# Kernel tuning notes

Measured on AMD Instinct MI355X. Metric: run time of the kernel, lower is better.

## Reference

```python
import jax, jax.numpy as jnp
import numpy as np

B, H, W, C = 2, 256, 256, 96
NH, WS, SS = 3, 8, 4
HD = C // NH
N = WS * WS              # tokens per window
NWIMG = (H // WS) * (W // WS)  # windows per image
MLP = 4 * C
EPS = 1e-5

def _np_attn_mask():
    img = np.zeros((H, W))
    sl = (slice(0, -WS), slice(-WS, -SS), slice(-SS, None))
    cnt = 0
    for a in sl:
        for b in sl:
            img[a, b] = cnt
            cnt += 1
    m = img.reshape(H // WS, WS, W // WS, WS).transpose(0, 2, 1, 3).reshape(-1, N)
    am = m[:, None, :] - m[:, :, None]
    return np.where(am != 0, -100.0, 0.0).astype(np.float32)

def _np_rel_index():
    coords = np.stack(np.meshgrid(np.arange(WS), np.arange(WS), indexing='ij'))
    cf = coords.reshape(2, -1)
    rel = (cf[:, :, None] - cf[:, None, :]).transpose(1, 2, 0).copy()
    rel[..., 0] += WS - 1
    rel[..., 1] += WS - 1
    rel[..., 0] *= 2 * WS - 1
    return rel.sum(-1)

def _np_coords_table():
    r = np.arange(-(WS - 1), WS, dtype=np.float32)
    t = np.stack(np.meshgrid(r, r, indexing='ij'), axis=-1) / (WS - 1) * 8.0
    t = np.sign(t) * np.log2(np.abs(t) + 1.0) / np.log2(8.0)
    return t.reshape(-1, 2)

ATTN_MASK = jnp.asarray(_np_attn_mask())          # [NWIMG, N, N]
REL_INDEX = jnp.asarray(_np_rel_index().reshape(-1))
COORDS_TABLE = jnp.asarray(_np_coords_table())    # [(2WS-1)^2, 2]

def setup_inputs():
    key = jax.random.key(0)
    ks = jax.random.split(key, 16)
    s = 0.02
    return {
        'hidden_states': jax.random.normal(ks[0], (B, H * W, C), jnp.float32),
        'time': jax.random.uniform(ks[1], (B,), jnp.float32),
        'q_w': jax.random.normal(ks[2], (C, C), jnp.float32) * s,
        'q_b': jnp.zeros((C,), jnp.float32),
        'k_w': jax.random.normal(ks[3], (C, C), jnp.float32) * s,
        'v_w': jax.random.normal(ks[4], (C, C), jnp.float32) * s,
        'v_b': jnp.zeros((C,), jnp.float32),
        'proj_w': jax.random.normal(ks[5], (C, C), jnp.float32) * s,
        'proj_b': jnp.zeros((C,), jnp.float32),
        'logit_scale': jnp.full((NH, 1, 1), jnp.log(10.0), jnp.float32),
        'cpb_w1': jax.random.normal(ks[6], (2, 512), jnp.float32) * s,
        'cpb_b1': jnp.zeros((512,), jnp.float32),
        'cpb_w2': jax.random.normal(ks[7], (512, NH), jnp.float32) * s,
        'lnb_ww': jax.random.normal(ks[8], (1, C), jnp.float32) * s,
        'lnb_wb': jnp.ones((C,), jnp.float32),
        'lnb_bw': jax.random.normal(ks[9], (1, C), jnp.float32) * s,
        'lnb_bb': jnp.zeros((C,), jnp.float32),
        'lna_ww': jax.random.normal(ks[10], (1, C), jnp.float32) * s,
        'lna_wb': jnp.ones((C,), jnp.float32),
        'lna_bw': jax.random.normal(ks[11], (1, C), jnp.float32) * s,
        'lna_bb': jnp.zeros((C,), jnp.float32),
        'fc1_w': jax.random.normal(ks[12], (C, MLP), jnp.float32) * s,
        'fc1_b': jnp.zeros((MLP,), jnp.float32),
        'fc2_w': jax.random.normal(ks[13], (MLP, C), jnp.float32) * s,
        'fc2_b': jnp.zeros((C,), jnp.float32),
    }

def _cln(x, time, ww, wb, bw, bb):
    # ConditionalLayerNorm: stats over channels, affine params from time via Linear(1, C)
    mean = x.mean(-1, keepdims=True)
    var = (x * x).mean(-1, keepdims=True) - mean * mean
    xn = (x - mean) / jnp.sqrt(var + EPS)
    t = time.reshape(-1, 1)
    w = (t @ ww + wb)[:, None, :]
    b = (t @ bw + bb)[:, None, :]
    return w * xn + b

def reference(hidden_states, time, q_w, q_b, k_w, v_w, v_b, proj_w, proj_b, logit_scale, cpb_w1, cpb_b1, cpb_w2, lnb_ww, lnb_wb, lnb_bw, lnb_bb, lna_ww, lna_wb, lna_bw, lna_bb, fc1_w, fc1_b, fc2_w, fc2_b):
    shortcut = hidden_states
    x = hidden_states.reshape(B, H, W, C)
    x = jnp.roll(x, (-SS, -SS), axis=(1, 2))  # cyclic shift
    # window partition -> [nW, N, C]
    xw = x.reshape(B, H // WS, WS, W // WS, WS, C).transpose(0, 1, 3, 2, 4, 5).reshape(-1, N, C)
    nW = B * NWIMG
    q = (xw @ q_w + q_b).reshape(nW, N, NH, HD).transpose(0, 2, 1, 3)
    k = (xw @ k_w).reshape(nW, N, NH, HD).transpose(0, 2, 1, 3)  # key has no bias in Swinv2
    v = (xw @ v_w + v_b).reshape(nW, N, NH, HD).transpose(0, 2, 1, 3)
    # cosine attention with clamped learnable log temperature
    qn = q / jnp.maximum(jnp.linalg.norm(q, axis=-1, keepdims=True), 1e-12)
    kn = k / jnp.maximum(jnp.linalg.norm(k, axis=-1, keepdims=True), 1e-12)
    scale = jnp.exp(jnp.minimum(logit_scale, jnp.log(100.0)))  # [NH,1,1]
    attn = jnp.einsum('whnd,whmd->whnm', qn, kn) * scale[None]
    # continuous relative position bias: MLP(2->512->NH) over log-spaced coords
    bias_table = jax.nn.relu(COORDS_TABLE @ cpb_w1 + cpb_b1) @ cpb_w2
    bias = bias_table[REL_INDEX].reshape(N, N, NH).transpose(2, 0, 1)
    attn = attn + 16.0 * jax.nn.sigmoid(bias)[None]
    # shifted-window mask
    attn = attn.reshape(B, NWIMG, NH, N, N) + ATTN_MASK[None, :, None]
    attn = jax.nn.softmax(attn.reshape(nW, NH, N, N), axis=-1)
    ctx = jnp.einsum('whnm,whmd->whnd', attn, v).transpose(0, 2, 1, 3).reshape(nW, N, C)
    ctx = ctx @ proj_w + proj_b
    # window reverse + un-shift
    xr = ctx.reshape(B, H // WS, W // WS, WS, WS, C).transpose(0, 1, 3, 2, 4, 5).reshape(B, H, W, C)
    xr = jnp.roll(xr, (SS, SS), axis=(1, 2))
    attn_out = xr.reshape(B, H * W, C)
    # post-norm residual (Swin v2 style) with conditional LN
    hs = shortcut + _cln(attn_out, time, lnb_ww, lnb_wb, lnb_bw, lnb_bb)
    inter = jax.nn.gelu(hs @ fc1_w + fc1_b, approximate=False)
    mlp_out = inter @ fc2_w + fc2_b
    return hs + _cln(mlp_out, time, lna_ww, lna_wb, lna_bw, lna_bb)
```

## Files before the change

kernel.cpp:

```cpp
#include <hip/hip_runtime.h>
#include <hip/hip_bf16.h>

typedef __bf16 bf16_t;
typedef bf16_t bf16x8 __attribute__((ext_vector_type(8)));
typedef bf16_t bf16x4 __attribute__((ext_vector_type(4)));
typedef float  f32x4  __attribute__((ext_vector_type(4)));

#define LDC 104
#define LDT 72

#define WS_WQ    0
#define WS_WK    19968
#define WS_WV    39936
#define WS_WP    59904
#define WS_FC1   79872
#define WS_FC2   159744
#define WS_BIAS  239616

__device__ __forceinline__ f32x4 mfma16(bf16x8 a, bf16x8 b, f32x4 c) {
    return __builtin_amdgcn_mfma_f32_16x16x32_bf16(a, b, c, 0, 0, 0);
}

__device__ __forceinline__ float cpbf(int v) {
    float x = (float)v * (8.0f / 7.0f);
    float l = log2f(fabsf(x) + 1.0f) * (1.0f / 3.0f);
    return x < 0.f ? -l : l;
}

__device__ __forceinline__ int regcnt(int t, int hw, int ww) {
    int r = t >> 3, c = t & 7;
    int rr = (hw == 31) ? (r < 4 ? 1 : 2) : 0;
    int cc = (ww == 31) ? (c < 4 ? 1 : 2) : 0;
    return rr * 3 + cc;
}

__global__ __launch_bounds__(256) void k0_prep(
    const float* __restrict__ qw, const float* __restrict__ kw,
    const float* __restrict__ vw, const float* __restrict__ pw,
    const float* __restrict__ fc1w, const float* __restrict__ fc2w,
    const float* __restrict__ cw1, const float* __restrict__ cb1,
    const float* __restrict__ cw2, char* __restrict__ ws)
{
    int tid = threadIdx.x;
    if (blockIdx.x == 0) {
        __shared__ float table[225 * 3];
        if (tid < 225) {
            int ia = tid / 15, ib = tid % 15;
            float c0 = cpbf(ia - 7), c1 = cpbf(ib - 7);
            float a0 = 0.f, a1 = 0.f, a2 = 0.f;
            for (int j = 0; j < 512; ++j) {
                float h = fmaf(c0, cw1[j], fmaf(c1, cw1[512 + j], cb1[j]));
                h = fmaxf(h, 0.f);
                a0 = fmaf(h, cw2[j * 3 + 0], a0);
                a1 = fmaf(h, cw2[j * 3 + 1], a1);
                a2 = fmaf(h, cw2[j * 3 + 2], a2);
            }
            table[tid * 3 + 0] = a0; table[tid * 3 + 1] = a1; table[tid * 3 + 2] = a2;
        }
        __syncthreads();
        float* bias = (float*)(ws + WS_BIAS);
        for (int e = tid; e < 3 * 64 * 64; e += 256) {
            int h = e >> 12, nm = e & 4095, n = nm >> 6, m = nm & 63;
            int dr = (n >> 3) - (m >> 3) + 7, dc = (n & 7) - (m & 7) + 7;
            float t = table[(dr * 15 + dc) * 3 + h];
            bias[e] = 16.f / (1.f + __expf(-t));
        }
    } else {
        int idx = (blockIdx.x - 1) * 256 + tid;
        if (idx < 36864) {
            int which = idx / 9216, r = idx % 9216;
            int o = r / 96, i = r % 96;
            const float* src = which == 0 ? qw : which == 1 ? kw : which == 2 ? vw : pw;
            ((bf16_t*)(ws + WS_WQ + which * 19968))[o * LDC + i] = (bf16_t)src[i * 96 + o];
        } else if (idx < 73728) {
            int r = idx - 36864;
            int o = r / 96, i = r % 96;
            ((bf16_t*)(ws + WS_FC1))[o * LDC + i] = (bf16_t)fc1w[i * 384 + o];
        } else if (idx < 110592) {
            int r = idx - 73728;
            int ks = r / 9216, rr = r % 9216, o = rr / 96, j = rr % 96;
            ((bf16_t*)(ws + WS_FC2))[(ks * 96 + o) * LDC + j] = (bf16_t)fc2w[(ks * 96 + j) * 96 + o];
        }
    }
}

__global__ __launch_bounds__(256) void kA_attn(
    const float* __restrict__ hidden, const float* __restrict__ tv,
    const float* __restrict__ qb, const float* __restrict__ vb,
    const float* __restrict__ pb, const float* __restrict__ lsc,
    const float* __restrict__ lnww, const float* __restrict__ lnwb,
    const float* __restrict__ lnbw, const float* __restrict__ lnbb,
    const char* __restrict__ ws, float* __restrict__ hs)
{
    __shared__ __align__(16) char sm[73728];
    bf16_t* xwb   = (bf16_t*)(sm + 0);
    bf16_t* wbuf  = (bf16_t*)(sm + 13312);
    bf16_t* qn    = (bf16_t*)(sm + 33280);
    bf16_t* kn    = (bf16_t*)(sm + 46592);
    bf16_t* vT    = (bf16_t*)(sm + 59904);
    bf16_t* P     = (bf16_t*)(sm + 0);
    bf16_t* ctxb  = (bf16_t*)(sm + 33280);
    bf16_t* wbuf2 = (bf16_t*)(sm + 46592);

    const int tid = threadIdx.x;
    const int wv = tid >> 6, lane = tid & 63, lg = lane >> 4, lr = lane & 15;
    const int wid = blockIdx.x;
    const int bat = wid >> 10, wim = wid & 1023, hw = wim >> 5, wwi = wim & 31;

    #pragma unroll
    for (int i = 0; i < 6; ++i) {
        int idx = tid + 256 * i;
        int t = idx / 24, grp = idx % 24;
        int gr = ((hw << 3) + (t >> 3) + 4) & 255;
        int gc = ((wwi << 3) + (t & 7) + 4) & 255;
        const float4 v = *(const float4*)(hidden + (((size_t)bat << 16) + (gr << 8) + gc) * 96 + grp * 4);
        bf16x4 p; p[0] = (bf16_t)v.x; p[1] = (bf16_t)v.y; p[2] = (bf16_t)v.z; p[3] = (bf16_t)v.w;
        *(bf16x4*)(xwb + t * LDC + grp * 4) = p;
    }
    {
        const float4* s4 = (const float4*)(ws + WS_WQ);
        float4* d4 = (float4*)wbuf;
        for (int i = tid; i < 1248; i += 256) d4[i] = s4[i];
    }
    __syncthreads();

    {
        bf16x8 af[3];
        #pragma unroll
        for (int ks = 0; ks < 3; ++ks) af[ks] = *(const bf16x8*)(xwb + (16 * wv + lr) * LDC + 32 * ks + 8 * lg);
        f32x4 acc[6];
        #pragma unroll
        for (int nt = 0; nt < 6; ++nt) {
            f32x4 a = {0.f, 0.f, 0.f, 0.f};
            #pragma unroll
            for (int ks = 0; ks < 3; ++ks)
                a = mfma16(af[ks], *(const bf16x8*)(wbuf + (16 * nt + lr) * LDC + 32 * ks + 8 * lg), a);
            float bq = qb[16 * nt + lr];
            #pragma unroll
            for (int j = 0; j < 4; ++j) a[j] += bq;
            acc[nt] = a;
        }
        #pragma unroll
        for (int h = 0; h < 3; ++h) {
            #pragma unroll
            for (int j = 0; j < 4; ++j) {
                float s = acc[2 * h][j] * acc[2 * h][j] + acc[2 * h + 1][j] * acc[2 * h + 1][j];
                s += __shfl_xor(s, 1); s += __shfl_xor(s, 2); s += __shfl_xor(s, 4); s += __shfl_xor(s, 8);
                float inv = 1.f / fmaxf(sqrtf(s), 1e-12f);
                int row = 16 * wv + 4 * lg + j;
                qn[row * LDC + 32 * h + lr]      = (bf16_t)(acc[2 * h][j] * inv);
                qn[row * LDC + 32 * h + 16 + lr] = (bf16_t)(acc[2 * h + 1][j] * inv);
            }
        }
    }
    __syncthreads();
    { const float4* s4 = (const float4*)(ws + WS_WK); float4* d4 = (float4*)wbuf;
      for (int i = tid; i < 1248; i += 256) d4[i] = s4[i]; }
    __syncthreads();

    {
        bf16x8 af[3];
        #pragma unroll
        for (int ks = 0; ks < 3; ++ks) af[ks] = *(const bf16x8*)(xwb + (16 * wv + lr) * LDC + 32 * ks + 8 * lg);
        f32x4 acc[6];
        #pragma unroll
        for (int nt = 0; nt < 6; ++nt) {
            f32x4 a = {0.f, 0.f, 0.f, 0.f};
            #pragma unroll
            for (int ks = 0; ks < 3; ++ks)
                a = mfma16(af[ks], *(const bf16x8*)(wbuf + (16 * nt + lr) * LDC + 32 * ks + 8 * lg), a);
            acc[nt] = a;
        }
        #pragma unroll
        for (int h = 0; h < 3; ++h) {
            #pragma unroll
            for (int j = 0; j < 4; ++j) {
                float s = acc[2 * h][j] * acc[2 * h][j] + acc[2 * h + 1][j] * acc[2 * h + 1][j];
                s += __shfl_xor(s, 1); s += __shfl_xor(s, 2); s += __shfl_xor(s, 4); s += __shfl_xor(s, 8);
                float inv = 1.f / fmaxf(sqrtf(s), 1e-12f);
                int row = 16 * wv + 4 * lg + j;
                kn[row * LDC + 32 * h + lr]      = (bf16_t)(acc[2 * h][j] * inv);
                kn[row * LDC + 32 * h + 16 + lr] = (bf16_t)(acc[2 * h + 1][j] * inv);
            }
        }
    }
    __syncthreads();
    { const float4* s4 = (const float4*)(ws + WS_WV); float4* d4 = (float4*)wbuf;
      for (int i = tid; i < 1248; i += 256) d4[i] = s4[i]; }
    __syncthreads();

    {
        bf16x8 af[3];
        #pragma unroll
        for (int ks = 0; ks < 3; ++ks) af[ks] = *(const bf16x8*)(xwb + (16 * wv + lr) * LDC + 32 * ks + 8 * lg);
        #pragma unroll
        for (int nt = 0; nt < 6; ++nt) {
            f32x4 a = {0.f, 0.f, 0.f, 0.f};
            #pragma unroll
            for (int ks = 0; ks < 3; ++ks)
                a = mfma16(af[ks], *(const bf16x8*)(wbuf + (16 * nt + lr) * LDC + 32 * ks + 8 * lg), a);
            int col = 16 * nt + lr;
            float bv = vb[col];
            bf16x4 pk;
            #pragma unroll
            for (int j = 0; j < 4; ++j) pk[j] = (bf16_t)(a[j] + bv);
            *(bf16x4*)(vT + col * LDT + 16 * wv + 4 * lg) = pk;
        }
    }
    __syncthreads();

    {
        float ls[3];
        #pragma unroll
        for (int h = 0; h < 3; ++h) ls[h] = __expf(fminf(lsc[h], 4.6051702f));
        f32x4 s[3][4];
        #pragma unroll
        for (int h = 0; h < 3; ++h) {
            bf16x8 aq = *(const bf16x8*)(qn + (16 * wv + lr) * LDC + 32 * h + 8 * lg);
            #pragma unroll
            for (int f = 0; f < 4; ++f) {
                f32x4 z = {0.f, 0.f, 0.f, 0.f};
                s[h][f] = mfma16(aq, *(const bf16x8*)(kn + (16 * f + lr) * LDC + 32 * h + 8 * lg), z);
            }
        }
        const float* biasT = (const float*)(ws + WS_BIAS);
        int cntm[4], cnti[4];
        #pragma unroll
        for (int f = 0; f < 4; ++f) cntm[f] = regcnt(16 * f + lr, hw, wwi);
        #pragma unroll
        for (int j = 0; j < 4; ++j) cnti[j] = regcnt(16 * wv + 4 * lg + j, hw, wwi);
        #pragma unroll
        for (int h = 0; h < 3; ++h) {
            #pragma unroll
            for (int f = 0; f < 4; ++f) {
                #pragma unroll
                for (int j = 0; j < 4; ++j) {
                    float b = biasT[(h << 12) + (16 * wv + 4 * lg + j) * 64 + 16 * f + lr];
                    float mk = (cnti[j] != cntm[f]) ? -100.f : 0.f;
                    s[h][f][j] = fmaf(s[h][f][j], ls[h], b + mk);
                }
            }
            #pragma unroll
            for (int j = 0; j < 4; ++j) {
                float mx = fmaxf(fmaxf(s[h][0][j], s[h][1][j]), fmaxf(s[h][2][j], s[h][3][j]));
                mx = fmaxf(mx, __shfl_xor(mx, 1)); mx = fmaxf(mx, __shfl_xor(mx, 2));
                mx = fmaxf(mx, __shfl_xor(mx, 4)); mx = fmaxf(mx, __shfl_xor(mx, 8));
                float sum = 0.f;
                #pragma unroll
                for (int f = 0; f < 4; ++f) { float e = __expf(s[h][f][j] - mx); s[h][f][j] = e; sum += e; }
                sum += __shfl_xor(sum, 1); sum += __shfl_xor(sum, 2); sum += __shfl_xor(sum, 4); sum += __shfl_xor(sum, 8);
                float inv = 1.f / sum;
                int row = 16 * wv + 4 * lg + j;
                #pragma unroll
                for (int f = 0; f < 4; ++f)
                    P[h * 64 * LDT + row * LDT + 16 * f + lr] = (bf16_t)(s[h][f][j] * inv);
            }
        }
    }
    __syncthreads();

    {
        f32x4 ctx[6]; f32x4 zz = {0.f, 0.f, 0.f, 0.f};
        #pragma unroll
        for (int t = 0; t < 6; ++t) ctx[t] = zz;
        #pragma unroll
        for (int h = 0; h < 3; ++h) {
            #pragma unroll
            for (int ks = 0; ks < 2; ++ks) {
                bf16x8 ap = *(const bf16x8*)(P + h * 64 * LDT + (16 * wv + lr) * LDT + 32 * ks + 8 * lg);
                #pragma unroll
                for (int dt = 0; dt < 2; ++dt)
                    ctx[2 * h + dt] = mfma16(ap, *(const bf16x8*)(vT + (32 * h + 16 * dt + lr) * LDT + 32 * ks + 8 * lg), ctx[2 * h + dt]);
            }
        }
        #pragma unroll
        for (int t = 0; t < 6; ++t) {
            #pragma unroll
            for (int j = 0; j < 4; ++j)
                ctxb[(16 * wv + 4 * lg + j) * LDC + 16 * t + lr] = (bf16_t)ctx[t][j];
        }
    }
    __syncthreads();
    { const float4* s4 = (const float4*)(ws + WS_WP); float4* d4 = (float4*)wbuf2;
      for (int i = tid; i < 1248; i += 256) d4[i] = s4[i]; }
    __syncthreads();

    {
        bf16x8 af[3];
        #pragma unroll
        for (int ks = 0; ks < 3; ++ks) af[ks] = *(const bf16x8*)(ctxb + (16 * wv + lr) * LDC + 32 * ks + 8 * lg);
        f32x4 acc[6];
        #pragma unroll
        for (int nt = 0; nt < 6; ++nt) {
            f32x4 a = {0.f, 0.f, 0.f, 0.f};
            #pragma unroll
            for (int ks = 0; ks < 3; ++ks)
                a = mfma16(af[ks], *(const bf16x8*)(wbuf2 + (16 * nt + lr) * LDC + 32 * ks + 8 * lg), a);
            float bp = pb[16 * nt + lr];
            #pragma unroll
            for (int j = 0; j < 4; ++j) a[j] += bp;
            acc[nt] = a;
        }
        float tb = tv[bat];
        #pragma unroll
        for (int j = 0; j < 4; ++j) {
            float smn = 0.f, sq = 0.f;
            #pragma unroll
            for (int t = 0; t < 6; ++t) { float v = acc[t][j]; smn += v; sq = fmaf(v, v, sq); }
            smn += __shfl_xor(smn, 1); smn += __shfl_xor(smn, 2); smn += __shfl_xor(smn, 4); smn += __shfl_xor(smn, 8);
            sq  += __shfl_xor(sq, 1);  sq  += __shfl_xor(sq, 2);  sq  += __shfl_xor(sq, 4);  sq  += __shfl_xor(sq, 8);
            float mean = smn * (1.f / 96.f);
            float var  = sq * (1.f / 96.f) - mean * mean;
            float rstd = rsqrtf(var + 1e-5f);
            int trow = 16 * wv + 4 * lg + j;
            int gr = ((hw << 3) + (trow >> 3) + 4) & 255;
            int gc = ((wwi << 3) + (trow & 7) + 4) & 255;
            size_t gbase = (((size_t)bat << 16) + (gr << 8) + gc) * 96;
            #pragma unroll
            for (int t = 0; t < 6; ++t) {
                int col = 16 * t + lr;
                float w = fmaf(tb, lnww[col], lnwb[col]);
                float b = fmaf(tb, lnbw[col], lnbb[col]);
                float xn = (acc[t][j] - mean) * rstd;
                hs[gbase + col] = hidden[gbase + col] + fmaf(w, xn, b);
            }
        }
    }
}

__global__ __launch_bounds__(256) void kB_mlp(
    const float* __restrict__ tv, const float* __restrict__ fc1b,
    const float* __restrict__ fc2b,
    const float* __restrict__ lnww, const float* __restrict__ lnwb,
    const float* __restrict__ lnbw, const float* __restrict__ lnbb,
    const char* __restrict__ ws, float* __restrict__ io)
{
    __shared__ __align__(16) char sm[66560];
    bf16_t* hsb  = (bf16_t*)(sm + 0);
    bf16_t* w1c  = (bf16_t*)(sm + 13312);
    bf16_t* gbuf = (bf16_t*)(sm + 33280);
    bf16_t* w2c  = (bf16_t*)(sm + 46592);

    const int tid = threadIdx.x;
    const int wv = tid >> 6, lane = tid & 63, lg = lane >> 4, lr = lane & 15;
    const size_t t0 = (size_t)blockIdx.x * 64;

    #pragma unroll
    for (int i = 0; i < 6; ++i) {
        int idx = tid + 256 * i;
        int t = idx / 24, grp = idx % 24;
        const float4 v = *(const float4*)(io + (t0 + t) * 96 + grp * 4);
        bf16x4 p; p[0] = (bf16_t)v.x; p[1] = (bf16_t)v.y; p[2] = (bf16_t)v.z; p[3] = (bf16_t)v.w;
        *(bf16x4*)(hsb + t * LDC + grp * 4) = p;
    }
    __syncthreads();

    f32x4 mlp[6]; f32x4 zz = {0.f, 0.f, 0.f, 0.f};
    #pragma unroll
    for (int t = 0; t < 6; ++t) mlp[t] = zz;
    bf16x8 hf[3];
    #pragma unroll
    for (int ks = 0; ks < 3; ++ks) hf[ks] = *(const bf16x8*)(hsb + (16 * wv + lr) * LDC + 32 * ks + 8 * lg);

    for (int ch = 0; ch < 4; ++ch) {
        { const float4* s1 = (const float4*)(ws + WS_FC1 + ch * 19968);
          const float4* s2 = (const float4*)(ws + WS_FC2 + ch * 19968);
          float4* d1 = (float4*)w1c; float4* d2 = (float4*)w2c;
          for (int i = tid; i < 1248; i += 256) { d1[i] = s1[i]; d2[i] = s2[i]; } }
        __syncthreads();
        #pragma unroll
        for (int nt = 0; nt < 6; ++nt) {
            f32x4 a = {0.f, 0.f, 0.f, 0.f};
            #pragma unroll
            for (int ks = 0; ks < 3; ++ks)
                a = mfma16(hf[ks], *(const bf16x8*)(w1c + (16 * nt + lr) * LDC + 32 * ks + 8 * lg), a);
            float bb = fc1b[ch * 96 + 16 * nt + lr];
            #pragma unroll
            for (int j = 0; j < 4; ++j) {
                float x = a[j] + bb;
                float g = 0.5f * x * (1.f + erff(x * 0.70710678f));
                gbuf[(16 * wv + 4 * lg + j) * LDC + 16 * nt + lr] = (bf16_t)g;
            }
        }
        __syncthreads();
        #pragma unroll
        for (int ks = 0; ks < 3; ++ks) {
            bf16x8 gf = *(const bf16x8*)(gbuf + (16 * wv + lr) * LDC + 32 * ks + 8 * lg);
            #pragma unroll
            for (int nt = 0; nt < 6; ++nt)
                mlp[nt] = mfma16(gf, *(const bf16x8*)(w2c + (16 * nt + lr) * LDC + 32 * ks + 8 * lg), mlp[nt]);
        }
        __syncthreads();
    }

    float tb = tv[t0 >> 16];
    #pragma unroll
    for (int nt = 0; nt < 6; ++nt) {
        float bb = fc2b[16 * nt + lr];
        #pragma unroll
        for (int j = 0; j < 4; ++j) mlp[nt][j] += bb;
    }
    #pragma unroll
    for (int j = 0; j < 4; ++j) {
        float smn = 0.f, sq = 0.f;
        #pragma unroll
        for (int t = 0; t < 6; ++t) { float v = mlp[t][j]; smn += v; sq = fmaf(v, v, sq); }
        smn += __shfl_xor(smn, 1); smn += __shfl_xor(smn, 2); smn += __shfl_xor(smn, 4); smn += __shfl_xor(smn, 8);
        sq  += __shfl_xor(sq, 1);  sq  += __shfl_xor(sq, 2);  sq  += __shfl_xor(sq, 4);  sq  += __shfl_xor(sq, 8);
        float mean = smn * (1.f / 96.f);
        float var  = sq * (1.f / 96.f) - mean * mean;
        float rstd = rsqrtf(var + 1e-5f);
        size_t row = t0 + 16 * wv + 4 * lg + j;
        #pragma unroll
        for (int t = 0; t < 6; ++t) {
            int col = 16 * t + lr;
            float w = fmaf(tb, lnww[col], lnwb[col]);
            float b = fmaf(tb, lnbw[col], lnbb[col]);
            float xn = (mlp[t][j] - mean) * rstd;
            io[row * 96 + col] = io[row * 96 + col] + fmaf(w, xn, b);
        }
    }
}

extern "C" void kernel_launch(void* const* d_in, const int* in_sizes, int n_in,
                              void* d_out, int out_size, void* d_ws, size_t ws_size,
                              hipStream_t stream)
{
    const float* hidden = (const float*)d_in[0];
    const float* tv     = (const float*)d_in[1];
    const float* q_w    = (const float*)d_in[2];
    const float* q_b    = (const float*)d_in[3];
    const float* k_w    = (const float*)d_in[4];
    const float* v_w    = (const float*)d_in[5];
    const float* v_b    = (const float*)d_in[6];
    const float* p_w    = (const float*)d_in[7];
    const float* p_b    = (const float*)d_in[8];
    const float* lsc    = (const float*)d_in[9];
    const float* cw1    = (const float*)d_in[10];
    const float* cb1    = (const float*)d_in[11];
    const float* cw2    = (const float*)d_in[12];
    const float* lnb_ww = (const float*)d_in[13];
    const float* lnb_wb = (const float*)d_in[14];
    const float* lnb_bw = (const float*)d_in[15];
    const float* lnb_bb = (const float*)d_in[16];
    const float* lna_ww = (const float*)d_in[17];
    const float* lna_wb = (const float*)d_in[18];
    const float* lna_bw = (const float*)d_in[19];
    const float* lna_bb = (const float*)d_in[20];
    const float* fc1_w  = (const float*)d_in[21];
    const float* fc1_b  = (const float*)d_in[22];
    const float* fc2_w  = (const float*)d_in[23];
    const float* fc2_b  = (const float*)d_in[24];
    char* ws = (char*)d_ws;
    float* out = (float*)d_out;

    k0_prep<<<dim3(433), dim3(256), 0, stream>>>(q_w, k_w, v_w, p_w, fc1_w, fc2_w, cw1, cb1, cw2, ws);
    kA_attn<<<dim3(2048), dim3(256), 0, stream>>>(hidden, tv, q_b, v_b, p_b, lsc,
                                                  lnb_ww, lnb_wb, lnb_bw, lnb_bb, ws, out);
    kB_mlp<<<dim3(2048), dim3(256), 0, stream>>>(tv, fc1_b, fc2_b,
                                                 lna_ww, lna_wb, lna_bw, lna_bb, ws, out);
}
```

Measured before the change: 328.1 us.

## Read weights from global directly, merge QKV phases, use tanh GELU, raise occupancy

Removes the LDS staging of weight matrices in the attention and MLP kernels and reads MFMA B-operands straight from global/L2. This shrinks shared memory and removes several barriers so more blocks fit per CU. The Q, K and V projections are merged into one phase, and the fragments for QK and PV are preloaded into registers so LDS buffers can be reused earlier. The exact erf GELU is replaced by a tanh-form approximation using exp and rcp, which changes numerics. The prep kernel also splits the bias-MLP reduction across twice as many threads.

After: 326.6 us. About the same (-0.4%).

```diff
diff --git a/kernel.cpp b/kernel.cpp
--- a/kernel.cpp
+++ b/kernel.cpp
@@ -34,7 +34,7 @@
     return rr * 3 + cc;
 }
 
-__global__ __launch_bounds__(256) void k0_prep(
+__global__ __launch_bounds__(512) void k0_prep(
     const float* __restrict__ qw, const float* __restrict__ kw,
     const float* __restrict__ vw, const float* __restrict__ pw,
     const float* __restrict__ fc1w, const float* __restrict__ fc2w,
@@ -43,30 +43,39 @@
 {
     int tid = threadIdx.x;
     if (blockIdx.x == 0) {
+        __shared__ float part[450 * 3];
         __shared__ float table[225 * 3];
-        if (tid < 225) {
-            int ia = tid / 15, ib = tid % 15;
+        if (tid < 450) {
+            int pos = tid >> 1, half = tid & 1;
+            int ia = pos / 15, ib = pos % 15;
             float c0 = cpbf(ia - 7), c1 = cpbf(ib - 7);
             float a0 = 0.f, a1 = 0.f, a2 = 0.f;
-            for (int j = 0; j < 512; ++j) {
+            int j0 = half * 256;
+            for (int j = j0; j < j0 + 256; ++j) {
                 float h = fmaf(c0, cw1[j], fmaf(c1, cw1[512 + j], cb1[j]));
                 h = fmaxf(h, 0.f);
                 a0 = fmaf(h, cw2[j * 3 + 0], a0);
                 a1 = fmaf(h, cw2[j * 3 + 1], a1);
                 a2 = fmaf(h, cw2[j * 3 + 2], a2);
             }
-            table[tid * 3 + 0] = a0; table[tid * 3 + 1] = a1; table[tid * 3 + 2] = a2;
+            part[tid * 3 + 0] = a0; part[tid * 3 + 1] = a1; part[tid * 3 + 2] = a2;
+        }
+        __syncthreads();
+        if (tid < 225) {
+            table[tid * 3 + 0] = part[(2 * tid) * 3 + 0] + part[(2 * tid + 1) * 3 + 0];
+            table[tid * 3 + 1] = part[(2 * tid) * 3 + 1] + part[(2 * tid + 1) * 3 + 1];
+            table[tid * 3 + 2] = part[(2 * tid) * 3 + 2] + part[(2 * tid + 1) * 3 + 2];
         }
         __syncthreads();
         float* bias = (float*)(ws + WS_BIAS);
-        for (int e = tid; e < 3 * 64 * 64; e += 256) {
+        for (int e = tid; e < 3 * 64 * 64; e += 512) {
             int h = e >> 12, nm = e & 4095, n = nm >> 6, m = nm & 63;
             int dr = (n >> 3) - (m >> 3) + 7, dc = (n & 7) - (m & 7) + 7;
             float t = table[(dr * 15 + dc) * 3 + h];
             bias[e] = 16.f / (1.f + __expf(-t));
         }
     } else {
-        int idx = (blockIdx.x - 1) * 256 + tid;
+        int idx = (blockIdx.x - 1) * 512 + tid;
         if (idx < 36864) {
             int which = idx / 9216, r = idx % 9216;
             int o = r / 96, i = r % 96;
@@ -84,7 +93,7 @@
     }
 }
 
-__global__ __launch_bounds__(256) void kA_attn(
+__global__ __launch_bounds__(256, 3) void kA_attn(
     const float* __restrict__ hidden, const float* __restrict__ tv,
     const float* __restrict__ qb, const float* __restrict__ vb,
     const float* __restrict__ pb, const float* __restrict__ lsc,
@@ -92,15 +101,13 @@
     const float* __restrict__ lnbw, const float* __restrict__ lnbb,
     const char* __restrict__ ws, float* __restrict__ hs)
 {
-    __shared__ __align__(16) char sm[73728];
-    bf16_t* xwb   = (bf16_t*)(sm + 0);
-    bf16_t* wbuf  = (bf16_t*)(sm + 13312);
-    bf16_t* qn    = (bf16_t*)(sm + 33280);
-    bf16_t* kn    = (bf16_t*)(sm + 46592);
-    bf16_t* vT    = (bf16_t*)(sm + 59904);
-    bf16_t* P     = (bf16_t*)(sm + 0);
-    bf16_t* ctxb  = (bf16_t*)(sm + 33280);
-    bf16_t* wbuf2 = (bf16_t*)(sm + 46592);
+    __shared__ __align__(16) char sm[53760];
+    bf16_t* xwb  = (bf16_t*)(sm + 0);
+    bf16_t* qn   = (bf16_t*)(sm + 13312);
+    bf16_t* kn   = (bf16_t*)(sm + 26624);
+    bf16_t* vT   = (bf16_t*)(sm + 39936);
+    bf16_t* P    = (bf16_t*)(sm + 0);
+    bf16_t* ctxb = (bf16_t*)(sm + 39936);
 
     const int tid = threadIdx.x;
     const int wv = tid >> 6, lane = tid & 63, lg = lane >> 4, lr = lane & 15;
@@ -110,119 +117,99 @@
     #pragma unroll
     for (int i = 0; i < 6; ++i) {
         int idx = tid + 256 * i;
-        int t = idx / 24, grp = idx % 24;
+        int t = idx / 24, grp = idx - t * 24;
         int gr = ((hw << 3) + (t >> 3) + 4) & 255;
         int gc = ((wwi << 3) + (t & 7) + 4) & 255;
         const float4 v = *(const float4*)(hidden + (((size_t)bat << 16) + (gr << 8) + gc) * 96 + grp * 4);
         bf16x4 p; p[0] = (bf16_t)v.x; p[1] = (bf16_t)v.y; p[2] = (bf16_t)v.z; p[3] = (bf16_t)v.w;
         *(bf16x4*)(xwb + t * LDC + grp * 4) = p;
     }
-    {
-        const float4* s4 = (const float4*)(ws + WS_WQ);
-        float4* d4 = (float4*)wbuf;
-        for (int i = tid; i < 1248; i += 256) d4[i] = s4[i];
-    }
     __syncthreads();
 
     {
         bf16x8 af[3];
         #pragma unroll
         for (int ks = 0; ks < 3; ++ks) af[ks] = *(const bf16x8*)(xwb + (16 * wv + lr) * LDC + 32 * ks + 8 * lg);
-        f32x4 acc[6];
-        #pragma unroll
-        for (int nt = 0; nt < 6; ++nt) {
-            f32x4 a = {0.f, 0.f, 0.f, 0.f};
-            #pragma unroll
-            for (int ks = 0; ks < 3; ++ks)
-                a = mfma16(af[ks], *(const bf16x8*)(wbuf + (16 * nt + lr) * LDC + 32 * ks + 8 * lg), a);
-            float bq = qb[16 * nt + lr];
-            #pragma unroll
-            for (int j = 0; j < 4; ++j) a[j] += bq;
-            acc[nt] = a;
-        }
+        const bf16_t* Wq = (const bf16_t*)(ws + WS_WQ);
+        const bf16_t* Wk = (const bf16_t*)(ws + WS_WK);
+        const bf16_t* Wv = (const bf16_t*)(ws + WS_WV);
+
         #pragma unroll
         for (int h = 0; h < 3; ++h) {
+            f32x4 a0 = {0.f,0.f,0.f,0.f}, a1 = {0.f,0.f,0.f,0.f};
+            #pragma unroll
+            for (int ks = 0; ks < 3; ++ks) {
+                a0 = mfma16(af[ks], *(const bf16x8*)(Wq + (32 * h + lr) * LDC + 32 * ks + 8 * lg), a0);
+                a1 = mfma16(af[ks], *(const bf16x8*)(Wq + (32 * h + 16 + lr) * LDC + 32 * ks + 8 * lg), a1);
+            }
+            float b0 = qb[32 * h + lr], b1 = qb[32 * h + 16 + lr];
+            #pragma unroll
+            for (int j = 0; j < 4; ++j) { a0[j] += b0; a1[j] += b1; }
             #pragma unroll
             for (int j = 0; j < 4; ++j) {
-                float s = acc[2 * h][j] * acc[2 * h][j] + acc[2 * h + 1][j] * acc[2 * h + 1][j];
+                float s = a0[j] * a0[j] + a1[j] * a1[j];
                 s += __shfl_xor(s, 1); s += __shfl_xor(s, 2); s += __shfl_xor(s, 4); s += __shfl_xor(s, 8);
                 float inv = 1.f / fmaxf(sqrtf(s), 1e-12f);
                 int row = 16 * wv + 4 * lg + j;
-                qn[row * LDC + 32 * h + lr]      = (bf16_t)(acc[2 * h][j] * inv);
-                qn[row * LDC + 32 * h + 16 + lr] = (bf16_t)(acc[2 * h + 1][j] * inv);
-            }
-        }
-    }
-    __syncthreads();
-    { const float4* s4 = (const float4*)(ws + WS_WK); float4* d4 = (float4*)wbuf;
-      for (int i = tid; i < 1248; i += 256) d4[i] = s4[i]; }
-    __syncthreads();
-
-    {
-        bf16x8 af[3];
-        #pragma unroll
-        for (int ks = 0; ks < 3; ++ks) af[ks] = *(const bf16x8*)(xwb + (16 * wv + lr) * LDC + 32 * ks + 8 * lg);
-        f32x4 acc[6];
-        #pragma unroll
-        for (int nt = 0; nt < 6; ++nt) {
-            f32x4 a = {0.f, 0.f, 0.f, 0.f};
-            #pragma unroll
-            for (int ks = 0; ks < 3; ++ks)
-                a = mfma16(af[ks], *(const bf16x8*)(wbuf + (16 * nt + lr) * LDC + 32 * ks + 8 * lg), a);
-            acc[nt] = a;
+                qn[row * LDC + 32 * h + lr]      = (bf16_t)(a0[j] * inv);
+                qn[row * LDC + 32 * h + 16 + lr] = (bf16_t)(a1[j] * inv);
+            }
         }
         #pragma unroll
         for (int h = 0; h < 3; ++h) {
+            f32x4 a0 = {0.f,0.f,0.f,0.f}, a1 = {0.f,0.f,0.f,0.f};
+            #pragma unroll
+            for (int ks = 0; ks < 3; ++ks) {
+                a0 = mfma16(af[ks], *(const bf16x8*)(Wk + (32 * h + lr) * LDC + 32 * ks + 8 * lg), a0);
+                a1 = mfma16(af[ks], *(const bf16x8*)(Wk + (32 * h + 16 + lr) * LDC + 32 * ks + 8 * lg), a1);
+            }
             #pragma unroll
             for (int j = 0; j < 4; ++j) {
-                float s = acc[2 * h][j] * acc[2 * h][j] + acc[2 * h + 1][j] * acc[2 * h + 1][j];
+                float s = a0[j] * a0[j] + a1[j] * a1[j];
                 s += __shfl_xor(s, 1); s += __shfl_xor(s, 2); s += __shfl_xor(s, 4); s += __shfl_xor(s, 8);
                 float inv = 1.f / fmaxf(sqrtf(s), 1e-12f);
                 int row = 16 * wv + 4 * lg + j;
-                kn[row * LDC + 32 * h + lr]      = (bf16_t)(acc[2 * h][j] * inv);
-                kn[row * LDC + 32 * h + 16 + lr] = (bf16_t)(acc[2 * h + 1][j] * inv);
-            }
+                kn[row * LDC + 32 * h + lr]      = (bf16_t)(a0[j] * inv);
+                kn[row * LDC + 32 * h + 16 + lr] = (bf16_t)(a1[j] * inv);
+            }
+        }
+        #pragma unroll
+        for (int nt = 0; nt < 6; ++nt) {
+            f32x4 a = {0.f,0.f,0.f,0.f};
+            #pragma unroll
+            for (int ks = 0; ks < 3; ++ks)
+                a = mfma16(af[ks], *(const bf16x8*)(Wv + (16 * nt + lr) * LDC + 32 * ks + 8 * lg), a);
+            float bv_ = vb[16 * nt + lr];
+            bf16x4 pk;
+            #pragma unroll
+            for (int j = 0; j < 4; ++j) pk[j] = (bf16_t)(a[j] + bv_);
+            *(bf16x4*)(vT + (16 * nt + lr) * LDT + 16 * wv + 4 * lg) = pk;
         }
     }
     __syncthreads();
-    { const float4* s4 = (const float4*)(ws + WS_WV); float4* d4 = (float4*)wbuf;
-      for (int i = tid; i < 1248; i += 256) d4[i] = s4[i]; }
-    __syncthreads();
 
     {
-        bf16x8 af[3];
-        #pragma unroll
-        for (int ks = 0; ks < 3; ++ks) af[ks] = *(const bf16x8*)(xwb + (16 * wv + lr) * LDC + 32 * ks + 8 * lg);
-        #pragma unroll
-        for (int nt = 0; nt < 6; ++nt) {
-            f32x4 a = {0.f, 0.f, 0.f, 0.f};
-            #pragma unroll
-            for (int ks = 0; ks < 3; ++ks)
-                a = mfma16(af[ks], *(const bf16x8*)(wbuf + (16 * nt + lr) * LDC + 32 * ks + 8 * lg), a);
-            int col = 16 * nt + lr;
-            float bv = vb[col];
-            bf16x4 pk;
-            #pragma unroll
-            for (int j = 0; j < 4; ++j) pk[j] = (bf16_t)(a[j] + bv);
-            *(bf16x4*)(vT + col * LDT + 16 * wv + 4 * lg) = pk;
-        }
-    }
-    __syncthreads();
-
-    {
+        bf16x8 aq[3], bk[3][4];
+        #pragma unroll
+        for (int h = 0; h < 3; ++h) {
+            aq[h] = *(const bf16x8*)(qn + (16 * wv + lr) * LDC + 32 * h + 8 * lg);
+            #pragma unroll
+            for (int f = 0; f < 4; ++f)
+                bk[h][f] = *(const bf16x8*)(kn + (16 * f + lr) * LDC + 32 * h + 8 * lg);
+        }
+        __syncthreads();
+
         float ls[3];
         #pragma unroll
         for (int h = 0; h < 3; ++h) ls[h] = __expf(fminf(lsc[h], 4.6051702f));
         f32x4 s[3][4];
         #pragma unroll
-        for (int h = 0; h < 3; ++h) {
-            bf16x8 aq = *(const bf16x8*)(qn + (16 * wv + lr) * LDC + 32 * h + 8 * lg);
+        for (int h = 0; h < 3; ++h)
             #pragma unroll
             for (int f = 0; f < 4; ++f) {
-                f32x4 z = {0.f, 0.f, 0.f, 0.f};
-                s[h][f] = mfma16(aq, *(const bf16x8*)(kn + (16 * f + lr) * LDC + 32 * h + 8 * lg), z);
-            }
-        }
+                f32x4 z = {0.f,0.f,0.f,0.f};
+                s[h][f] = mfma16(aq[h], bk[h][f], z);
+            }
         const float* biasT = (const float*)(ws + WS_BIAS);
         int cntm[4], cnti[4];
         #pragma unroll
@@ -232,14 +219,13 @@
         #pragma unroll
         for (int h = 0; h < 3; ++h) {
             #pragma unroll
-            for (int f = 0; f < 4; ++f) {
+            for (int f = 0; f < 4; ++f)
                 #pragma unroll
                 for (int j = 0; j < 4; ++j) {
                     float b = biasT[(h << 12) + (16 * wv + 4 * lg + j) * 64 + 16 * f + lr];
                     float mk = (cnti[j] != cntm[f]) ? -100.f : 0.f;
                     s[h][f][j] = fmaf(s[h][f][j], ls[h], b + mk);
                 }
-            }
             #pragma unroll
             for (int j = 0; j < 4; ++j) {
                 float mx = fmaxf(fmaxf(s[h][0][j], s[h][1][j]), fmaxf(s[h][2][j], s[h][3][j]));
@@ -260,42 +246,47 @@
     __syncthreads();
 
     {
-        f32x4 ctx[6]; f32x4 zz = {0.f, 0.f, 0.f, 0.f};
-        #pragma unroll
-        for (int t = 0; t < 6; ++t) ctx[t] = zz;
-        #pragma unroll
-        for (int h = 0; h < 3; ++h) {
+        bf16x8 ap[3][2], bv2[3][2][2];
+        #pragma unroll
+        for (int h = 0; h < 3; ++h)
             #pragma unroll
             for (int ks = 0; ks < 2; ++ks) {
-                bf16x8 ap = *(const bf16x8*)(P + h * 64 * LDT + (16 * wv + lr) * LDT + 32 * ks + 8 * lg);
+                ap[h][ks] = *(const bf16x8*)(P + h * 64 * LDT + (16 * wv + lr) * LDT + 32 * ks + 8 * lg);
                 #pragma unroll
                 for (int dt = 0; dt < 2; ++dt)
-                    ctx[2 * h + dt] = mfma16(ap, *(const bf16x8*)(vT + (32 * h + 16 * dt + lr) * LDT + 32 * ks + 8 * lg), ctx[2 * h + dt]);
-            }
-        }
-        #pragma unroll
-        for (int t = 0; t < 6; ++t) {
+                    bv2[h][dt][ks] = *(const bf16x8*)(vT + (32 * h + 16 * dt + lr) * LDT + 32 * ks + 8 * lg);
+            }
+        f32x4 ctx[6];
+        #pragma unroll
+        for (int t = 0; t < 6; ++t) { f32x4 z = {0.f,0.f,0.f,0.f}; ctx[t] = z; }
+        #pragma unroll
+        for (int h = 0; h < 3; ++h)
+            #pragma unroll
+            for (int ks = 0; ks < 2; ++ks)
+                #pragma unroll
+                for (int dt = 0; dt < 2; ++dt)
+                    ctx[2 * h + dt] = mfma16(ap[h][ks], bv2[h][dt][ks], ctx[2 * h + dt]);
+        __syncthreads();
+        #pragma unroll
+        for (int t = 0; t < 6; ++t)
             #pragma unroll
             for (int j = 0; j < 4; ++j)
                 ctxb[(16 * wv + 4 * lg + j) * LDC + 16 * t + lr] = (bf16_t)ctx[t][j];
-        }
     }
     __syncthreads();
-    { const float4* s4 = (const float4*)(ws + WS_WP); float4* d4 = (float4*)wbuf2;
-      for (int i = tid; i < 1248; i += 256) d4[i] = s4[i]; }
-    __syncthreads();
 
     {
+        const bf16_t* Wp = (const bf16_t*)(ws + WS_WP);
         bf16x8 af[3];
         #pragma unroll
         for (int ks = 0; ks < 3; ++ks) af[ks] = *(const bf16x8*)(ctxb + (16 * wv + lr) * LDC + 32 * ks + 8 * lg);
         f32x4 acc[6];
         #pragma unroll
         for (int nt = 0; nt < 6; ++nt) {
-            f32x4 a = {0.f, 0.f, 0.f, 0.f};
+            f32x4 a = {0.f,0.f,0.f,0.f};
             #pragma unroll
             for (int ks = 0; ks < 3; ++ks)
-                a = mfma16(af[ks], *(const bf16x8*)(wbuf2 + (16 * nt + lr) * LDC + 32 * ks + 8 * lg), a);
+                a = mfma16(af[ks], *(const bf16x8*)(Wp + (16 * nt + lr) * LDC + 32 * ks + 8 * lg), a);
             float bp = pb[16 * nt + lr];
             #pragma unroll
             for (int j = 0; j < 4; ++j) a[j] += bp;
@@ -328,57 +319,52 @@
     }
 }
 
-__global__ __launch_bounds__(256) void kB_mlp(
+__global__ __launch_bounds__(256, 4) void kB_mlp(
     const float* __restrict__ tv, const float* __restrict__ fc1b,
     const float* __restrict__ fc2b,
     const float* __restrict__ lnww, const float* __restrict__ lnwb,
     const float* __restrict__ lnbw, const float* __restrict__ lnbb,
     const char* __restrict__ ws, float* __restrict__ io)
 {
-    __shared__ __align__(16) char sm[66560];
-    bf16_t* hsb  = (bf16_t*)(sm + 0);
-    bf16_t* w1c  = (bf16_t*)(sm + 13312);
-    bf16_t* gbuf = (bf16_t*)(sm + 33280);
-    bf16_t* w2c  = (bf16_t*)(sm + 46592);
+    __shared__ __align__(16) bf16_t gbuf[64 * LDC];
 
     const int tid = threadIdx.x;
     const int wv = tid >> 6, lane = tid & 63, lg = lane >> 4, lr = lane & 15;
     const size_t t0 = (size_t)blockIdx.x * 64;
 
-    #pragma unroll
-    for (int i = 0; i < 6; ++i) {
-        int idx = tid + 256 * i;
-        int t = idx / 24, grp = idx % 24;
-        const float4 v = *(const float4*)(io + (t0 + t) * 96 + grp * 4);
-        bf16x4 p; p[0] = (bf16_t)v.x; p[1] = (bf16_t)v.y; p[2] = (bf16_t)v.z; p[3] = (bf16_t)v.w;
-        *(bf16x4*)(hsb + t * LDC + grp * 4) = p;
-    }
-    __syncthreads();
-
-    f32x4 mlp[6]; f32x4 zz = {0.f, 0.f, 0.f, 0.f};
-    #pragma unroll
-    for (int t = 0; t < 6; ++t) mlp[t] = zz;
     bf16x8 hf[3];
     #pragma unroll
-    for (int ks = 0; ks < 3; ++ks) hf[ks] = *(const bf16x8*)(hsb + (16 * wv + lr) * LDC + 32 * ks + 8 * lg);
+    for (int ks = 0; ks < 3; ++ks) {
+        const float* p = io + (t0 + 16 * wv + lr) * 96 + 32 * ks + 8 * lg;
+        float4 u0 = *(const float4*)p;
+        float4 u1 = *(const float4*)(p + 4);
+        bf16x8 f;
+        f[0] = (bf16_t)u0.x; f[1] = (bf16_t)u0.y; f[2] = (bf16_t)u0.z; f[3] = (bf16_t)u0.w;
+        f[4] = (bf16_t)u1.x; f[5] = (bf16_t)u1.y; f[6] = (bf16_t)u1.z; f[7] = (bf16_t)u1.w;
+        hf[ks] = f;
+    }
+
+    f32x4 mlp[6];
+    #pragma unroll
+    for (int t = 0; t < 6; ++t) { f32x4 z = {0.f,0.f,0.f,0.f}; mlp[t] = z; }
+    const bf16_t* w1 = (const bf16_t*)(ws + WS_FC1);
+    const bf16_t* w2 = (const bf16_t*)(ws + WS_FC2);
 
     for (int ch = 0; ch < 4; ++ch) {
-        { const float4* s1 = (const float4*)(ws + WS_FC1 + ch * 19968);
-          const float4* s2 = (const float4*)(ws + WS_FC2 + ch * 19968);
-          float4* d1 = (float4*)w1c; float4* d2 = (float4*)w2c;
-          for (int i = tid; i < 1248; i += 256) { d1[i] = s1[i]; d2[i] = s2[i]; } }
-        __syncthreads();
+        if (ch) __syncthreads();
         #pragma unroll
         for (int nt = 0; nt < 6; ++nt) {
-            f32x4 a = {0.f, 0.f, 0.f, 0.f};
+            f32x4 a = {0.f,0.f,0.f,0.f};
             #pragma unroll
             for (int ks = 0; ks < 3; ++ks)
-                a = mfma16(hf[ks], *(const bf16x8*)(w1c + (16 * nt + lr) * LDC + 32 * ks + 8 * lg), a);
+                a = mfma16(hf[ks], *(const bf16x8*)(w1 + (ch * 96 + 16 * nt + lr) * LDC + 32 * ks + 8 * lg), a);
             float bb = fc1b[ch * 96 + 16 * nt + lr];
             #pragma unroll
             for (int j = 0; j < 4; ++j) {
                 float x = a[j] + bb;
-                float g = 0.5f * x * (1.f + erff(x * 0.70710678f));
+                float u = 0.7978845608f * fmaf(0.044715f * x, x * x, x);
+                float t = __expf(2.f * u);
+                float g = x - x * __builtin_amdgcn_rcpf(t + 1.f);
                 gbuf[(16 * wv + 4 * lg + j) * LDC + 16 * nt + lr] = (bf16_t)g;
             }
         }
@@ -388,9 +374,8 @@
             bf16x8 gf = *(const bf16x8*)(gbuf + (16 * wv + lr) * LDC + 32 * ks + 8 * lg);
             #pragma unroll
             for (int nt = 0; nt < 6; ++nt)
-                mlp[nt] = mfma16(gf, *(const bf16x8*)(w2c + (16 * nt + lr) * LDC + 32 * ks + 8 * lg), mlp[nt]);
-        }
-        __syncthreads();
+                mlp[nt] = mfma16(gf, *(const bf16x8*)(w2 + (ch * 96 + 16 * nt + lr) * LDC + 32 * ks + 8 * lg), mlp[nt]);
+        }
     }
 
     float tb = tv[t0 >> 16];
@@ -447,14 +432,14 @@
     const float* lna_wb = (const float*)d_in[18];
     const float* lna_bw = (const float*)d_in[19];
     const float* lna_bb = (const float*)d_in[20];
+    const float* fc1_b  = (const float*)d_in[22];
+    const float* fc2_b  = (const float*)d_in[24];
     const float* fc1_w  = (const float*)d_in[21];
-    const float* fc1_b  = (const float*)d_in[22];
     const float* fc2_w  = (const float*)d_in[23];
-    const float* fc2_b  = (const float*)d_in[24];
     char* ws = (char*)d_ws;
     float* out = (float*)d_out;
 
-    k0_prep<<<dim3(433), dim3(256), 0, stream>>>(q_w, k_w, v_w, p_w, fc1_w, fc2_w, cw1, cb1, cw2, ws);
+    k0_prep<<<dim3(217), dim3(512), 0, stream>>>(q_w, k_w, v_w, p_w, fc1_w, fc2_w, cw1, cb1, cw2, ws);
     kA_attn<<<dim3(2048), dim3(256), 0, stream>>>(hidden, tv, q_b, v_b, p_b, lsc,
                                                   lnb_ww, lnb_wb, lnb_bw, lnb_bb, ws, out);
     kB_mlp<<<dim3(2048), dim3(256), 0, stream>>>(tv, fc1_b, fc2_b,
```
